# Performance work log

Hardware: AMD Instinct MI355X
Metric: run time of the kernel (lower is better)

The kernel has to match this reference:

```python
import jax, jax.numpy as jnp
import numpy as np

# Conv config matching init_kwargs
C_IN, C_OUT = 128, 256
KH, KW = 3, 3
STRIDE = (1, 1)
PADDING = ((1, 1), (1, 1))
DILATION = (1, 1)
B, H, W = 32, 56, 56


def setup_inputs() -> dict:
    key = jax.random.key(0)
    k1, k2, k3 = jax.random.split(key, 3)
    x = jax.random.normal(k1, (B, C_IN, H, W), dtype=jnp.float32)
    # Flattened weight as stored by Conv2DUF: conv.weight.view(O,-1).t() -> [C*kh*kw, O]
    weight = jax.random.normal(k2, (C_IN * KH * KW, C_OUT), dtype=jnp.float32) * 0.02
    bias = jax.random.normal(k3, (C_OUT,), dtype=jnp.float32) * 0.02
    return {"x": x, "weight": weight, "bias": bias}


def reference(x, weight, bias):
    # Conv2DUF computes unfold(x) @ weight + bias, which is exactly a 2D
    # cross-correlation with the original conv kernel. Recover the [O,C,kh,kw]
    # kernel from the flattened [C*kh*kw, O] matrix and use the fused conv
    # primitive (same math, no giant im2col buffer).
    kernel = weight.T.reshape(C_OUT, C_IN, KH, KW)
    out = jax.lax.conv_general_dilated(
        x, kernel,
        window_strides=STRIDE,
        padding=PADDING,
        rhs_dilation=DILATION,
        dimension_numbers=("NCHW", "OIHW", "NCHW"),
    )
    return out + bias[None, :, None, None]
```

## Files before the change

kernel.cpp:

```cpp
#include <hip/hip_runtime.h>
#include <stdint.h>


#define C_INQ 128
#define C_OUTQ 256
#define HDIM 56
#define WDIM 56
#define BDIM 32
#define HP 58
#define WP 58
#define HWPIX (HDIM * WDIM)
#define XT_ELEMS ((size_t)BDIM * HP * WP * C_INQ)
#define XT_BYTES (XT_ELEMS * 2)

typedef __bf16 bf16x8 __attribute__((ext_vector_type(8)));
typedef unsigned short ushort8 __attribute__((ext_vector_type(8)));
typedef float floatx4 __attribute__((ext_vector_type(4)));

__device__ __forceinline__ unsigned short f2bf(float f) {
  union { float f; unsigned int u; } v; v.f = f;
  unsigned int u = v.u;
  unsigned int r = u + 0x7FFFu + ((u >> 16) & 1u);
  return (unsigned short)(r >> 16);
}
__device__ __forceinline__ unsigned int pack2(float a, float b) {
  return (unsigned int)f2bf(a) | ((unsigned int)f2bf(b) << 16);
}

__global__ __launch_bounds__(256) void pad_transpose_kernel(
    const float* __restrict__ x, unsigned short* __restrict__ xt) {
  const int blk = blockIdx.x;
  const int b = blk / HP;
  const int hp = blk % HP;
  const int t = threadIdx.x;
  uint4* __restrict__ xtrow4 = (uint4*)(xt + (size_t)(b * HP + hp) * (WP * C_INQ));
  if (hp == 0 || hp == HP - 1) {
    for (int i = t; i < 928; i += 256) xtrow4[i] = make_uint4(0, 0, 0, 0);
    return;
  }
  __shared__ float lds[C_INQ * 62];
  const int h = hp - 1;
  const float* __restrict__ xb = x + (size_t)b * C_INQ * HWPIX + (size_t)h * WDIM;
  for (int i = t; i < 1792; i += 256) {
    int c = i / 14, w4 = (i - c * 14) * 4;
    const float4 v = *(const float4*)(xb + (size_t)c * HWPIX + w4);
    float* d = lds + c * 62 + w4;
    *(float2*)d = make_float2(v.x, v.y);
    *(float2*)(d + 2) = make_float2(v.z, v.w);
  }
  __syncthreads();
  for (int j = t; j < 928; j += 256) {
    int wp = j >> 4, c8 = (j & 15) * 8;
    uint4 o;
    if (wp == 0 || wp == WP - 1) {
      o = make_uint4(0, 0, 0, 0);
    } else {
      const float* s = lds + c8 * 62 + (wp - 1);
      o.x = pack2(s[0],   s[62]);
      o.y = pack2(s[124], s[186]);
      o.z = pack2(s[248], s[310]);
      o.w = pack2(s[372], s[434]);
    }
    xtrow4[j] = o;
  }
}

__global__ __launch_bounds__(256) void weight_transform_kernel(
    const float* __restrict__ w, unsigned short* __restrict__ wt) {
  const int bx = blockIdx.x;
  const int khw = bx >> 4;
  const int r4 = bx & 15;
  const int n0w = (r4 >> 2) * 64;
  const int c32 = (r4 & 3) * 32;
  const int t = threadIdx.x;
  __shared__ float lds[32 * 66];
#pragma unroll
  for (int r = 0; r < 8; ++r) {
    int idx = r * 256 + t;
    int n = idx & 63, c = idx >> 6;
    lds[c * 66 + n] = w[(size_t)((c32 + c) * 9 + khw) * C_OUTQ + n0w + n];
  }
  __syncthreads();
  {
    int n = t >> 2, c8 = (t & 3) * 8;
    const float* s = lds + c8 * 66 + n;
    uint4 o;
    o.x = pack2(s[0],   s[66]);
    o.y = pack2(s[132], s[198]);
    o.z = pack2(s[264], s[330]);
    o.w = pack2(s[396], s[462]);
    *(uint4*)(wt + (size_t)khw * (C_OUTQ * C_INQ) + (size_t)(n0w + n) * C_INQ + c32 + c8) = o;
  }
}

#define BM 128
#define BN 256
#define BK 64
#define STEPS 18

__global__ __launch_bounds__(256, 2) void conv_gemm_kernel(
    const unsigned short* __restrict__ xt,
    const unsigned short* __restrict__ wt,
    const float* __restrict__ bias,
    float* __restrict__ out) {
  __shared__ __align__(16) unsigned short ldsA[BM * BK];
  __shared__ __align__(16) unsigned short ldsB[BN * BK];

  const int t = threadIdx.x;
  const int lane = t & 63;
  const int wave = t >> 6;
  const int tile_m = blockIdx.x;

  int gbaseA[4], gbaseB[8];
#pragma unroll
  for (int r = 0; r < 4; ++r) {
    int g = r * 256 + t;
    int row = g >> 3;
    int kpart = (g & 7) ^ (row & 7);
    int pix = tile_m * BM + row;
    int b = pix / HWPIX;
    int p = pix - b * HWPIX;
    int h = p / WDIM;
    int w = p - h * WDIM;
    gbaseA[r] = ((b * HP + h) * WP + w) * C_INQ + kpart * 8;
  }
#pragma unroll
  for (int r = 0; r < 8; ++r) {
    int g = r * 256 + t;
    int row = g >> 3;
    int kpart = (g & 7) ^ (row & 7);
    gbaseB[r] = row * C_INQ + kpart * 8;
  }

  const int wm = (wave >> 1) * 64;
  const int wn = (wave & 1) * 128;
  const int mrow = lane & 15;
  const int quad = lane >> 4;
  const int xorv = mrow & 7;

  floatx4 acc[4][8] = {};

  for (int s = 0; s < STEPS; ++s) {
    const int khw = s >> 1;
    const int c0 = (s & 1) * 64;
    const int kh = khw / 3;
    const int kw = khw - kh * 3;
    const int koffA = (kh * WP + kw) * C_INQ + c0;
    const int koffB = khw * (C_OUTQ * C_INQ) + c0;
#pragma unroll
    for (int r = 0; r < 4; ++r)
      __builtin_amdgcn_global_load_lds(
          (const __attribute__((address_space(1))) unsigned int*)(xt + gbaseA[r] + koffA),
          (__attribute__((address_space(3))) unsigned int*)(ldsA + (r * 256 + wave * 64) * 8),
          16, 0, 0);
#pragma unroll
    for (int r = 0; r < 8; ++r)
      __builtin_amdgcn_global_load_lds(
          (const __attribute__((address_space(1))) unsigned int*)(wt + gbaseB[r] + koffB),
          (__attribute__((address_space(3))) unsigned int*)(ldsB + (r * 256 + wave * 64) * 8),
          16, 0, 0);
    __syncthreads();

#pragma unroll
    for (int u = 0; u < 2; ++u) {
      const int kx = ((u * 4 + quad) ^ xorv) * 8;
      bf16x8 afr[4], bfr[8];
#pragma unroll
      for (int i = 0; i < 4; ++i)
        afr[i] = __builtin_bit_cast(bf16x8,
                 *(const ushort8*)(ldsA + (wm + i * 16 + mrow) * 64 + kx));
#pragma unroll
      for (int jn = 0; jn < 8; ++jn)
        bfr[jn] = __builtin_bit_cast(bf16x8,
                  *(const ushort8*)(ldsB + (wn + jn * 16 + mrow) * 64 + kx));
#pragma unroll
      for (int i = 0; i < 4; ++i)
#pragma unroll
        for (int jn = 0; jn < 8; ++jn)
          acc[i][jn] = __builtin_amdgcn_mfma_f32_16x16x32_bf16(afr[i], bfr[jn], acc[i][jn], 0, 0, 0);
    }
    __syncthreads();
  }

  float bv[8];
#pragma unroll
  for (int jn = 0; jn < 8; ++jn) bv[jn] = bias[wn + jn * 16 + mrow];
#pragma unroll
  for (int i = 0; i < 4; ++i) {
    const int mbase = tile_m * BM + wm + i * 16 + quad * 4;
    const int b = mbase / HWPIX;
    const int p = mbase - b * HWPIX;
    float* obase = out + (size_t)b * (C_OUTQ * HWPIX) + p;
#pragma unroll
    for (int jn = 0; jn < 8; ++jn) {
      const int ng = wn + jn * 16 + mrow;
      floatx4 v = acc[i][jn];
      v[0] += bv[jn]; v[1] += bv[jn]; v[2] += bv[jn]; v[3] += bv[jn];
      *(floatx4*)(obase + (size_t)ng * HWPIX) = v;
    }
  }
}

extern "C" void kernel_launch(void* const* d_in, const int* in_sizes, int n_in,
                              void* d_out, int out_size, void* d_ws, size_t ws_size,
                              hipStream_t stream) {
  const float* x    = (const float*)d_in[0];
  const float* w    = (const float*)d_in[1];
  const float* bias = (const float*)d_in[2];
  float* out = (float*)d_out;

  unsigned short* xt = (unsigned short*)d_ws;
  unsigned short* wt = (unsigned short*)((char*)d_ws + XT_BYTES);

  hipLaunchKernelGGL(pad_transpose_kernel, dim3(BDIM * HP), dim3(256), 0, stream, x, xt);
  hipLaunchKernelGGL(weight_transform_kernel, dim3(144), dim3(256), 0, stream, w, wt);
  hipLaunchKernelGGL(conv_gemm_kernel, dim3(784), dim3(256), 0, stream, xt, wt, bias, out);
}
```

Before: 215.3 us.

## Triple-buffer LDS with BK=32 and channel-grouped input layout

Changes the padded input layout to 16 channel groups of 8 (group-major planes), rewrites the pad/transpose kernel to convert directly from registers without LDS, and halves BK to 32. It adds a three-stage LDS ring buffer with async global->LDS loads issued three steps ahead, using vmcnt waits and barriers, so memory latency overlaps MFMA work. The trade-offs are more barriers per unit of work, a strided global access pattern across the channel planes, and higher LDS use, which could limit occupancy.

```diff
diff --git a/kernel.cpp b/kernel.cpp
--- a/kernel.cpp
+++ b/kernel.cpp
@@ -10,7 +10,8 @@
 #define HP 58
 #define WP 58
 #define HWPIX (HDIM * WDIM)
-#define XT_ELEMS ((size_t)BDIM * HP * WP * C_INQ)
+#define GSTRIDE (BDIM * HP * WP * 8)
+#define XT_ELEMS ((size_t)16 * GSTRIDE)
 #define XT_BYTES (XT_ELEMS * 2)
 
 typedef __bf16 bf16x8 __attribute__((ext_vector_type(8)));
@@ -31,37 +32,43 @@
     const float* __restrict__ x, unsigned short* __restrict__ xt) {
   const int blk = blockIdx.x;
   const int b = blk / HP;
-  const int hp = blk % HP;
+  const int hp = blk - b * HP;
   const int t = threadIdx.x;
-  uint4* __restrict__ xtrow4 = (uint4*)(xt + (size_t)(b * HP + hp) * (WP * C_INQ));
+  uint4* __restrict__ xt4 = (uint4*)xt;
   if (hp == 0 || hp == HP - 1) {
-    for (int i = t; i < 928; i += 256) xtrow4[i] = make_uint4(0, 0, 0, 0);
+    for (int i = t; i < 16 * WP; i += 256) {
+      int g = i / WP, wp = i - g * WP;
+      xt4[((size_t)(g * BDIM + b) * HP + hp) * WP + wp] = make_uint4(0, 0, 0, 0);
+    }
     return;
   }
-  __shared__ float lds[C_INQ * 62];
   const int h = hp - 1;
-  const float* __restrict__ xb = x + (size_t)b * C_INQ * HWPIX + (size_t)h * WDIM;
-  for (int i = t; i < 1792; i += 256) {
-    int c = i / 14, w4 = (i - c * 14) * 4;
-    const float4 v = *(const float4*)(xb + (size_t)c * HWPIX + w4);
-    float* d = lds + c * 62 + w4;
-    *(float2*)d = make_float2(v.x, v.y);
-    *(float2*)(d + 2) = make_float2(v.z, v.w);
-  }
-  __syncthreads();
-  for (int j = t; j < 928; j += 256) {
-    int wp = j >> 4, c8 = (j & 15) * 8;
-    uint4 o;
-    if (wp == 0 || wp == WP - 1) {
-      o = make_uint4(0, 0, 0, 0);
-    } else {
-      const float* s = lds + c8 * 62 + (wp - 1);
-      o.x = pack2(s[0],   s[62]);
-      o.y = pack2(s[124], s[186]);
-      o.z = pack2(s[248], s[310]);
-      o.w = pack2(s[372], s[434]);
-    }
-    xtrow4[j] = o;
+  if (t < 224) {
+    const int g = t / 14;
+    const int w4 = (t - g * 14) * 4;
+    const float* xp = x + ((size_t)b * C_INQ + g * 8) * HWPIX + h * WDIM + w4;
+    float4 L0 = *(const float4*)(xp);
+    float4 L1 = *(const float4*)(xp + HWPIX);
+    float4 L2 = *(const float4*)(xp + 2 * HWPIX);
+    float4 L3 = *(const float4*)(xp + 3 * HWPIX);
+    float4 L4 = *(const float4*)(xp + 4 * HWPIX);
+    float4 L5 = *(const float4*)(xp + 5 * HWPIX);
+    float4 L6 = *(const float4*)(xp + 6 * HWPIX);
+    float4 L7 = *(const float4*)(xp + 7 * HWPIX);
+    uint4* dst = xt4 + ((size_t)(g * BDIM + b) * HP + hp) * WP + 1 + w4;
+    dst[0] = make_uint4(pack2(L0.x, L1.x), pack2(L2.x, L3.x),
+                        pack2(L4.x, L5.x), pack2(L6.x, L7.x));
+    dst[1] = make_uint4(pack2(L0.y, L1.y), pack2(L2.y, L3.y),
+                        pack2(L4.y, L5.y), pack2(L6.y, L7.y));
+    dst[2] = make_uint4(pack2(L0.z, L1.z), pack2(L2.z, L3.z),
+                        pack2(L4.z, L5.z), pack2(L6.z, L7.z));
+    dst[3] = make_uint4(pack2(L0.w, L1.w), pack2(L2.w, L3.w),
+                        pack2(L4.w, L5.w), pack2(L6.w, L7.w));
+  } else {
+    const int r = t - 224;
+    const int g = r >> 1;
+    const int wp = (r & 1) * (WP - 1);
+    xt4[((size_t)(g * BDIM + b) * HP + hp) * WP + wp] = make_uint4(0, 0, 0, 0);
   }
 }
 
@@ -95,40 +102,40 @@
 
 #define BM 128
 #define BN 256
-#define BK 64
-#define STEPS 18
+#define BK 32
+#define STEPS 36
 
 __global__ __launch_bounds__(256, 2) void conv_gemm_kernel(
     const unsigned short* __restrict__ xt,
     const unsigned short* __restrict__ wt,
     const float* __restrict__ bias,
     float* __restrict__ out) {
-  __shared__ __align__(16) unsigned short ldsA[BM * BK];
-  __shared__ __align__(16) unsigned short ldsB[BN * BK];
+  __shared__ __align__(16) unsigned short ldsA[3 * BM * BK];
+  __shared__ __align__(16) unsigned short ldsB[3 * BN * BK];
 
   const int t = threadIdx.x;
   const int lane = t & 63;
   const int wave = t >> 6;
   const int tile_m = blockIdx.x;
 
-  int gbaseA[4], gbaseB[8];
-#pragma unroll
-  for (int r = 0; r < 4; ++r) {
+  int gbaseA[2], gbaseB[4];
+#pragma unroll
+  for (int r = 0; r < 2; ++r) {
     int g = r * 256 + t;
-    int row = g >> 3;
-    int kpart = (g & 7) ^ (row & 7);
+    int row = g >> 2;
+    int kpart = (g & 3) ^ (row & 3);
     int pix = tile_m * BM + row;
     int b = pix / HWPIX;
     int p = pix - b * HWPIX;
     int h = p / WDIM;
     int w = p - h * WDIM;
-    gbaseA[r] = ((b * HP + h) * WP + w) * C_INQ + kpart * 8;
-  }
-#pragma unroll
-  for (int r = 0; r < 8; ++r) {
+    gbaseA[r] = kpart * GSTRIDE + ((b * HP + h) * WP + w) * 8;
+  }
+#pragma unroll
+  for (int r = 0; r < 4; ++r) {
     int g = r * 256 + t;
-    int row = g >> 3;
-    int kpart = (g & 7) ^ (row & 7);
+    int row = g >> 2;
+    int kpart = (g & 3) ^ (row & 3);
     gbaseB[r] = row * C_INQ + kpart * 8;
   }
 
@@ -136,51 +143,85 @@
   const int wn = (wave & 1) * 128;
   const int mrow = lane & 15;
   const int quad = lane >> 4;
-  const int xorv = mrow & 7;
+
+  int aoff[4], boff[8];
+#pragma unroll
+  for (int i = 0; i < 4; ++i) {
+    int row = wm + i * 16 + mrow;
+    aoff[i] = row * BK + ((quad ^ (row & 3)) * 8);
+  }
+#pragma unroll
+  for (int j = 0; j < 8; ++j) {
+    int row = wn + j * 16 + mrow;
+    boff[j] = row * BK + ((quad ^ (row & 3)) * 8);
+  }
+
+  const int ldst = wave * 64 * 8;
 
   floatx4 acc[4][8] = {};
 
-  for (int s = 0; s < STEPS; ++s) {
-    const int khw = s >> 1;
-    const int c0 = (s & 1) * 64;
+  auto stage = [&](int s2, int bufc) {
+    const int khw = s2 >> 2;
+    const int cq = s2 & 3;
     const int kh = khw / 3;
     const int kw = khw - kh * 3;
-    const int koffA = (kh * WP + kw) * C_INQ + c0;
-    const int koffB = khw * (C_OUTQ * C_INQ) + c0;
+    const int koffA = cq * 4 * GSTRIDE + (kh * WP + kw) * 8;
+    const int koffB = khw * (C_OUTQ * C_INQ) + cq * 32;
+#pragma unroll
+    for (int r = 0; r < 2; ++r)
+      __builtin_amdgcn_global_load_lds(
+          (const __attribute__((address_space(1))) unsigned int*)(xt + gbaseA[r] + koffA),
+          (__attribute__((address_space(3))) unsigned int*)(ldsA + bufc * (BM * BK) + r * 2048 + ldst),
+          16, 0, 0);
 #pragma unroll
     for (int r = 0; r < 4; ++r)
       __builtin_amdgcn_global_load_lds(
-          (const __attribute__((address_space(1))) unsigned int*)(xt + gbaseA[r] + koffA),
-          (__attribute__((address_space(3))) unsigned int*)(ldsA + (r * 256 + wave * 64) * 8),
+          (const __attribute__((address_space(1))) unsigned int*)(wt + gbaseB[r] + koffB),
+          (__attribute__((address_space(3))) unsigned int*)(ldsB + bufc * (BN * BK) + r * 2048 + ldst),
           16, 0, 0);
-#pragma unroll
-    for (int r = 0; r < 8; ++r)
-      __builtin_amdgcn_global_load_lds(
-          (const __attribute__((address_space(1))) unsigned int*)(wt + gbaseB[r] + koffB),
-          (__attribute__((address_space(3))) unsigned int*)(ldsB + (r * 256 + wave * 64) * 8),
-          16, 0, 0);
-    __syncthreads();
-
-#pragma unroll
-    for (int u = 0; u < 2; ++u) {
-      const int kx = ((u * 4 + quad) ^ xorv) * 8;
-      bf16x8 afr[4], bfr[8];
-#pragma unroll
-      for (int i = 0; i < 4; ++i)
-        afr[i] = __builtin_bit_cast(bf16x8,
-                 *(const ushort8*)(ldsA + (wm + i * 16 + mrow) * 64 + kx));
-#pragma unroll
-      for (int jn = 0; jn < 8; ++jn)
-        bfr[jn] = __builtin_bit_cast(bf16x8,
-                  *(const ushort8*)(ldsB + (wn + jn * 16 + mrow) * 64 + kx));
-#pragma unroll
-      for (int i = 0; i < 4; ++i)
-#pragma unroll
-        for (int jn = 0; jn < 8; ++jn)
-          acc[i][jn] = __builtin_amdgcn_mfma_f32_16x16x32_bf16(afr[i], bfr[jn], acc[i][jn], 0, 0, 0);
-    }
-    __syncthreads();
-  }
+  };
+
+  auto compute_step = [&](int bufc) {
+    const unsigned short* A = ldsA + bufc * (BM * BK);
+    const unsigned short* B = ldsB + bufc * (BN * BK);
+    bf16x8 afr[4], bfr[8];
+#pragma unroll
+    for (int i = 0; i < 4; ++i)
+      afr[i] = __builtin_bit_cast(bf16x8, *(const ushort8*)(A + aoff[i]));
+#pragma unroll
+    for (int j = 0; j < 8; ++j)
+      bfr[j] = __builtin_bit_cast(bf16x8, *(const ushort8*)(B + boff[j]));
+#pragma unroll
+    for (int i = 0; i < 4; ++i)
+#pragma unroll
+      for (int j = 0; j < 8; ++j)
+        acc[i][j] = __builtin_amdgcn_mfma_f32_16x16x32_bf16(afr[i], bfr[j], acc[i][j], 0, 0, 0);
+  };
+
+#define K_STEP(S, BUF, VM, DOSTAGE)                                  \
+  {                                                                  \
+    asm volatile("s_waitcnt vmcnt(" VM ")" ::: "memory");            \
+    __builtin_amdgcn_s_barrier();                                    \
+    compute_step(BUF);                                               \
+    __builtin_amdgcn_s_barrier();                                    \
+    if (DOSTAGE) stage((S) + 3, BUF);                                \
+  }
+
+  stage(0, 0);
+  stage(1, 1);
+  stage(2, 2);
+
+#pragma unroll 1
+  for (int so = 0; so < 11; ++so) {
+    const int s = so * 3;
+    K_STEP(s, 0, "12", true);
+    K_STEP(s + 1, 1, "12", true);
+    K_STEP(s + 2, 2, "12", true);
+  }
+  K_STEP(33, 0, "12", false);
+  K_STEP(34, 1, "6", false);
+  K_STEP(35, 2, "0", false);
+#undef K_STEP
 
   float bv[8];
 #pragma unroll
```

Measured after the change: 234.4 us. 8.9% more time.
